# Optimization experiments

Hardware: AMD Instinct MI355X
Metric: run time of the kernel (lower is better)

## Reference

```python
import jax, jax.numpy as jnp
import numpy as np

NUM_EXPERTS = 64
TOP_K = 2
NOISE_EPS = 0.01


def setup_inputs() -> dict:
    key = jax.random.key(0)
    k1, k2, k3, k4 = jax.random.split(key, 4)
    B, D, E = 32768, 2048, NUM_EXPERTS
    x = jax.random.normal(k1, (B, D), dtype=jnp.float32)
    # original inits these to zero; use small random weights for a non-degenerate top-k
    w_gate = jax.random.normal(k2, (D, E), dtype=jnp.float32) * 0.02
    w_noise = jax.random.normal(k3, (D, E), dtype=jnp.float32) * 0.02
    noise = jax.random.normal(k4, (B, E), dtype=jnp.float32)  # tf.random.normal draw, fixed
    return {"x": x, "w_gate": w_gate, "w_noise": w_noise, "noise": noise}


def reference(x, w_gate, w_noise, noise):
    # routing_pooling='flatten' on a 2D input is identity
    pooled = x  # [B, D]
    routing = pooled @ w_gate  # [B, E]
    # noisy routing (training=True path)
    noise_stddev = jax.nn.softplus(pooled @ w_noise) + NOISE_EPS
    routing = routing + noise * noise_stddev
    # softmax_top_k: take top k+1, keep top k, softmax, scatter back to E experts
    kk = min(TOP_K + 1, NUM_EXPERTS)
    top_vals, top_idx = jax.lax.top_k(routing, kk)
    top_k_vals = top_vals[:, :TOP_K]            # [B, k]
    top_k_idx = top_idx[:, :TOP_K]              # [B, k]
    top_k_gates = jax.nn.softmax(top_k_vals, axis=-1)
    B = routing.shape[0]
    rows = jnp.arange(B)[:, None]
    # rowwise_unsorted_segment_sum -> scatter gates into expert slots
    out = jnp.zeros((B, NUM_EXPERTS), dtype=routing.dtype).at[rows, top_k_idx].add(top_k_gates)
    return out
```

## Files before the change

### kernel.cpp

```cpp
#include <hip/hip_runtime.h>
#include <math.h>


typedef _Float16 half4v __attribute__((ext_vector_type(4)));
typedef _Float16 half8v __attribute__((ext_vector_type(8)));
typedef float f32x4 __attribute__((ext_vector_type(4)));

constexpr int DIMK = 2048;
constexpr int NEXP = 64;
constexpr int BM   = 64;
constexpr int NCH  = DIMK / 32;

__device__ __forceinline__ void async_load16(const void* g, void* l) {
    __builtin_amdgcn_global_load_lds(
        (const __attribute__((address_space(1))) unsigned int*)g,
        (__attribute__((address_space(3))) unsigned int*)l, 16, 0, 0);
}

__device__ __forceinline__ bool gt_pair(float a, int ia, float b, int ib) {
    return (a > b) || (a == b && ia < ib);
}

__global__ __launch_bounds__(256)
void presplit_kernel(const float* __restrict__ wg, const float* __restrict__ wn,
                     _Float16* __restrict__ wsB)
{
    int gid  = blockIdx.x * 256 + threadIdx.x;
    int lane = gid & 63;
    int t    = (gid >> 6) & 7;
    int c    = gid >> 9;
    int n    = t * 16 + (lane & 15);
    int kb   = c * 32 + ((lane >> 4) << 3);
    const float* src = (n < NEXP) ? (wg + n) : (wn + (n - NEXP));
    half8v h1, h2;
    #pragma unroll
    for (int j = 0; j < 8; ++j) {
        float w = src[(size_t)(kb + j) * NEXP] * 65536.0f;
        _Float16 a = (_Float16)w;
        h1[j] = a;
        h2[j] = (_Float16)(w - (float)a);
    }
    *(half8v*)(wsB + ((((size_t)c * 2 + 0) * 8 + t) * 64 + lane) * 8) = h1;
    *(half8v*)(wsB + ((((size_t)c * 2 + 1) * 8 + t) * 64 + lane) * 8) = h2;
}

__global__ __launch_bounds__(256)
void routing_mfma(const float* __restrict__ x, const _Float16* __restrict__ wsB,
                  const float* __restrict__ noise, float* __restrict__ out)
{
    __shared__ _Float16 Bp[4][2][8][64][8];
    __shared__ float4   cand[BM][2];
    __shared__ float4   res[BM];

    const int tid  = threadIdx.x;
    const int lane = tid & 63;
    const int w    = tid >> 6;
    const int wm   = w >> 1;
    const int wnh  = w & 1;
    const int q    = lane >> 4;
    const int cidx = lane & 15;
    const int row0 = blockIdx.x * BM;

    f32x4  acc[2][4] = {};
    float4 ra[2][4];

    const float* xr0 = x + (size_t)(row0 + wm * 32 + cidx) * DIMK + q * 8;
    const float* xr1 = xr0 + 16 * DIMK;

    auto issue_B = [&](int c, int buf) {
        #pragma unroll
        for (int ii = 0; ii < 4; ++ii) {
            int idx = w * 4 + ii;
            int p = idx >> 3, t = idx & 7;
            const _Float16* g = wsB + ((((size_t)c * 2 + p) * 8 + t) * 64 + lane) * 8;
            async_load16(g, &Bp[buf][p][t][0][0]);
        }
    };

#define ISSUE_A(C, S)                                            \
    {   const float* pa_ = xr0 + (C) * 32;                       \
        const float* pb_ = xr1 + (C) * 32;                       \
        ra[S][0] = *(const float4*)(pa_);                        \
        ra[S][1] = *(const float4*)(pa_ + 4);                    \
        ra[S][2] = *(const float4*)(pb_);                        \
        ra[S][3] = *(const float4*)(pb_ + 4);  }

#define FENCE() asm volatile("" ::: "memory")

#define STEP(C, BUF, NBUF, SEL, ISS, WN)                                     \
    {                                                                        \
        asm volatile("s_waitcnt vmcnt(" #WN ")" ::: "memory");               \
        asm volatile("s_barrier" ::: "memory");                              \
        if (ISS) issue_B((C) + 2, NBUF);                                     \
        half8v af[2][2];                                                     \
        _Pragma("unroll")                                                    \
        for (int mt = 0; mt < 2; ++mt) {                                     \
            _Pragma("unroll")                                                \
            for (int h = 0; h < 2; ++h) {                                    \
                float4 v = ra[SEL][mt * 2 + h];                              \
                float f0 = v.x * 1024.f, f1 = v.y * 1024.f;                  \
                float f2 = v.z * 1024.f, f3 = v.w * 1024.f;                  \
                _Float16 a0 = (_Float16)f0, a1 = (_Float16)f1;               \
                _Float16 a2 = (_Float16)f2, a3 = (_Float16)f3;               \
                af[mt][0][h * 4 + 0] = a0;                                   \
                af[mt][0][h * 4 + 1] = a1;                                   \
                af[mt][0][h * 4 + 2] = a2;                                   \
                af[mt][0][h * 4 + 3] = a3;                                   \
                af[mt][1][h * 4 + 0] = (_Float16)(f0 - (float)a0);           \
                af[mt][1][h * 4 + 1] = (_Float16)(f1 - (float)a1);           \
                af[mt][1][h * 4 + 2] = (_Float16)(f2 - (float)a2);           \
                af[mt][1][h * 4 + 3] = (_Float16)(f3 - (float)a3);           \
            }                                                                \
        }                                                                    \
        if (ISS) ISSUE_A((C) + 2, SEL);                                      \
        half8v bf[4][2];                                                     \
        _Pragma("unroll")                                                    \
        for (int tt = 0; tt < 4; ++tt) {                                     \
            int ntile = (tt < 2) ? (wnh * 2 + tt) : (4 + wnh * 2 + (tt - 2));\
            _Pragma("unroll")                                                \
            for (int p = 0; p < 2; ++p)                                      \
                bf[tt][p] = *(const half8v*)&Bp[BUF][p][ntile][lane][0];     \
        }                                                                    \
        _Pragma("unroll")                                                    \
        for (int mt = 0; mt < 2; ++mt) {                                     \
            _Pragma("unroll")                                                \
            for (int tt = 0; tt < 4; ++tt) {                                 \
                acc[mt][tt] = __builtin_amdgcn_mfma_f32_16x16x32_f16(        \
                    af[mt][0], bf[tt][0], acc[mt][tt], 0, 0, 0);             \
                acc[mt][tt] = __builtin_amdgcn_mfma_f32_16x16x32_f16(        \
                    af[mt][0], bf[tt][1], acc[mt][tt], 0, 0, 0);             \
                acc[mt][tt] = __builtin_amdgcn_mfma_f32_16x16x32_f16(        \
                    af[mt][1], bf[tt][0], acc[mt][tt], 0, 0, 0);             \
            }                                                                \
        }                                                                    \
    }

    issue_B(0, 0);
    ISSUE_A(0, 0);
    FENCE();
    issue_B(1, 1);
    ISSUE_A(1, 1);

    #pragma unroll 1
    for (int cb = 0; cb < NCH - 4; cb += 4) {
        STEP(cb + 0, 0, 2, 0, 1, 8)
        STEP(cb + 1, 1, 3, 1, 1, 8)
        STEP(cb + 2, 2, 0, 0, 1, 8)
        STEP(cb + 3, 3, 1, 1, 1, 8)
    }
    STEP(NCH - 4, 0, 2, 0, 1, 8)
    STEP(NCH - 3, 1, 3, 1, 1, 8)
    STEP(NCH - 2, 2, 0, 0, 0, 8)
    STEP(NCH - 1, 3, 0, 1, 0, 0)

#undef STEP
#undef ISSUE_A
#undef FENCE

    const float s = 0x1p-26f;
    #pragma unroll
    for (int mt = 0; mt < 2; ++mt) {
        float rv[2][4];
        #pragma unroll
        for (int g = 0; g < 2; ++g) {
            int e     = wnh * 32 + g * 16 + cidx;
            int rbase = row0 + wm * 32 + mt * 16 + q * 4;
            #pragma unroll
            for (int r = 0; r < 4; ++r) {
                float nz   = noise[(size_t)(rbase + r) * NEXP + e];
                float gate = acc[mt][g][r] * s;
                float nv   = acc[mt][g + 2][r] * s;
                float sp   = fmaxf(nv, 0.f) + log1pf(expf(-fabsf(nv)));
                rv[g][r]   = gate + nz * (sp + 0.01f);
            }
        }
        #pragma unroll
        for (int r = 0; r < 4; ++r) {
            int e0 = wnh * 32 + cidx, e1 = e0 + 16;
            float v1, v2; int i1, i2;
            float a = rv[0][r], b = rv[1][r];
            if (a >= b) { v1 = a; i1 = e0; v2 = b; i2 = e1; }
            else        { v1 = b; i1 = e1; v2 = a; i2 = e0; }
            #pragma unroll
            for (int m = 1; m <= 8; m <<= 1) {
                float b1 = __shfl_xor(v1, m); int ib1 = __shfl_xor(i1, m);
                float b2 = __shfl_xor(v2, m); int ib2 = __shfl_xor(i2, m);
                if (gt_pair(b1, ib1, v1, i1)) {
                    float o1 = v1; int oi1 = i1;
                    v1 = b1; i1 = ib1;
                    if (gt_pair(b2, ib2, o1, oi1)) { v2 = b2; i2 = ib2; }
                    else                           { v2 = o1; i2 = oi1; }
                } else if (gt_pair(b1, ib1, v2, i2)) {
                    v2 = b1; i2 = ib1;
                }
            }
            if (cidx == 0) {
                int rowb = wm * 32 + mt * 16 + q * 4 + r;
                cand[rowb][wnh] = make_float4(v1, __int_as_float(i1),
                                              v2, __int_as_float(i2));
            }
        }
    }
    __syncthreads();

    if (tid < BM) {
        float4 c0 = cand[tid][0], c1 = cand[tid][1];
        float mv1 = c0.x; int mi1 = __float_as_int(c0.y);
        float mv2 = c0.z; int mi2 = __float_as_int(c0.w);
        float b1 = c1.x;  int ib1 = __float_as_int(c1.y);
        float b2 = c1.z;  int ib2 = __float_as_int(c1.w);
        if (gt_pair(b1, ib1, mv1, mi1)) {
            float o1 = mv1; int oi1 = mi1;
            mv1 = b1; mi1 = ib1;
            if (gt_pair(b2, ib2, o1, oi1)) { mv2 = b2; mi2 = ib2; }
            else                           { mv2 = o1; mi2 = oi1; }
        } else if (gt_pair(b1, ib1, mv2, mi2)) {
            mv2 = b1; mi2 = ib1;
        }
        float t  = expf(mv2 - mv1);
        float g1 = 1.f / (1.f + t);
        res[tid] = make_float4(g1, __int_as_float(mi1),
                               t * g1, __int_as_float(mi2));
    }
    __syncthreads();

    {
        int rr  = tid >> 2;
        int seg = tid & 3;
        float4 rv = res[rr];
        float g1 = rv.x, g2 = rv.z;
        int   j1 = __float_as_int(rv.y), j2 = __float_as_int(rv.w);
        float* op = out + (size_t)(row0 + rr) * NEXP + seg * 16;
        #pragma unroll
        for (int qq = 0; qq < 4; ++qq) {
            int e0 = seg * 16 + qq * 4;
            float4 o;
            o.x = (e0 + 0 == j1) ? g1 : ((e0 + 0 == j2) ? g2 : 0.f);
            o.y = (e0 + 1 == j1) ? g1 : ((e0 + 1 == j2) ? g2 : 0.f);
            o.z = (e0 + 2 == j1) ? g1 : ((e0 + 2 == j2) ? g2 : 0.f);
            o.w = (e0 + 3 == j1) ? g1 : ((e0 + 3 == j2) ? g2 : 0.f);
            *(float4*)(op + qq * 4) = o;
        }
    }
}

extern "C" void kernel_launch(void* const* d_in, const int* in_sizes, int n_in,
                              void* d_out, int out_size, void* d_ws, size_t ws_size,
                              hipStream_t stream) {
    const float* x     = (const float*)d_in[0];
    const float* wg    = (const float*)d_in[1];
    const float* wn    = (const float*)d_in[2];
    const float* noise = (const float*)d_in[3];
    float* out = (float*)d_out;
    _Float16* wsB = (_Float16*)d_ws;

    presplit_kernel<<<dim3(128), 256, 0, stream>>>(wg, wn, wsB);

    const int Brows = in_sizes[0] / DIMK;
    dim3 grid(Brows / BM);
    routing_mfma<<<grid, 256, 0, stream>>>(x, wsB, noise, out);
}
```

Measured before the change: 419.3 us.

## Use 8 waves per block with one M-tile each and deeper prefetch

After: 403.3 us. 1.04x faster.

```diff
diff --git a/kernel.cpp b/kernel.cpp
--- a/kernel.cpp
+++ b/kernel.cpp
@@ -44,7 +44,7 @@
     *(half8v*)(wsB + ((((size_t)c * 2 + 1) * 8 + t) * 64 + lane) * 8) = h2;
 }
 
-__global__ __launch_bounds__(256)
+__global__ __launch_bounds__(512, 4)
 void routing_mfma(const float* __restrict__ x, const _Float16* __restrict__ wsB,
                   const float* __restrict__ noise, float* __restrict__ out)
 {
@@ -55,22 +55,21 @@
     const int tid  = threadIdx.x;
     const int lane = tid & 63;
     const int w    = tid >> 6;
-    const int wm   = w >> 1;
+    const int mt   = w >> 1;
     const int wnh  = w & 1;
     const int q    = lane >> 4;
     const int cidx = lane & 15;
     const int row0 = blockIdx.x * BM;
 
-    f32x4  acc[2][4] = {};
-    float4 ra[2][4];
-
-    const float* xr0 = x + (size_t)(row0 + wm * 32 + cidx) * DIMK + q * 8;
-    const float* xr1 = xr0 + 16 * DIMK;
+    f32x4  acc[4] = {};
+    float4 ra[4][2];
+
+    const float* xr0 = x + (size_t)(row0 + mt * 16 + cidx) * DIMK + q * 8;
 
     auto issue_B = [&](int c, int buf) {
         #pragma unroll
-        for (int ii = 0; ii < 4; ++ii) {
-            int idx = w * 4 + ii;
+        for (int ii = 0; ii < 2; ++ii) {
+            int idx = w * 2 + ii;
             int p = idx >> 3, t = idx & 7;
             const _Float16* g = wsB + ((((size_t)c * 2 + p) * 8 + t) * 64 + lane) * 8;
             async_load16(g, &Bp[buf][p][t][0][0]);
@@ -79,60 +78,46 @@
 
 #define ISSUE_A(C, S)                                            \
     {   const float* pa_ = xr0 + (C) * 32;                       \
-        const float* pb_ = xr1 + (C) * 32;                       \
         ra[S][0] = *(const float4*)(pa_);                        \
-        ra[S][1] = *(const float4*)(pa_ + 4);                    \
-        ra[S][2] = *(const float4*)(pb_);                        \
-        ra[S][3] = *(const float4*)(pb_ + 4);  }
+        ra[S][1] = *(const float4*)(pa_ + 4);  }
 
 #define FENCE() asm volatile("" ::: "memory")
 
-#define STEP(C, BUF, NBUF, SEL, ISS, WN)                                     \
+#define STEP(C, ISS, WN)                                                     \
     {                                                                        \
         asm volatile("s_waitcnt vmcnt(" #WN ")" ::: "memory");               \
         asm volatile("s_barrier" ::: "memory");                              \
-        if (ISS) issue_B((C) + 2, NBUF);                                     \
-        half8v af[2][2];                                                     \
+        if (ISS) issue_B((C) + 3, ((C) + 3) & 3);                            \
+        half8v af0, af1;                                                     \
         _Pragma("unroll")                                                    \
-        for (int mt = 0; mt < 2; ++mt) {                                     \
-            _Pragma("unroll")                                                \
-            for (int h = 0; h < 2; ++h) {                                    \
-                float4 v = ra[SEL][mt * 2 + h];                              \
-                float f0 = v.x * 1024.f, f1 = v.y * 1024.f;                  \
-                float f2 = v.z * 1024.f, f3 = v.w * 1024.f;                  \
-                _Float16 a0 = (_Float16)f0, a1 = (_Float16)f1;               \
-                _Float16 a2 = (_Float16)f2, a3 = (_Float16)f3;               \
-                af[mt][0][h * 4 + 0] = a0;                                   \
-                af[mt][0][h * 4 + 1] = a1;                                   \
-                af[mt][0][h * 4 + 2] = a2;                                   \
-                af[mt][0][h * 4 + 3] = a3;                                   \
-                af[mt][1][h * 4 + 0] = (_Float16)(f0 - (float)a0);           \
-                af[mt][1][h * 4 + 1] = (_Float16)(f1 - (float)a1);           \
-                af[mt][1][h * 4 + 2] = (_Float16)(f2 - (float)a2);           \
-                af[mt][1][h * 4 + 3] = (_Float16)(f3 - (float)a3);           \
-            }                                                                \
+        for (int h = 0; h < 2; ++h) {                                        \
+            float4 v = ra[(C) & 3][h];                                       \
+            float f0 = v.x * 1024.f, f1 = v.y * 1024.f;                      \
+            float f2 = v.z * 1024.f, f3 = v.w * 1024.f;                      \
+            _Float16 a0 = (_Float16)f0, a1 = (_Float16)f1;                   \
+            _Float16 a2 = (_Float16)f2, a3 = (_Float16)f3;                   \
+            af0[h * 4 + 0] = a0; af0[h * 4 + 1] = a1;                        \
+            af0[h * 4 + 2] = a2; af0[h * 4 + 3] = a3;                        \
+            af1[h * 4 + 0] = (_Float16)(f0 - (float)a0);                     \
+            af1[h * 4 + 1] = (_Float16)(f1 - (float)a1);                     \
+            af1[h * 4 + 2] = (_Float16)(f2 - (float)a2);                     \
+            af1[h * 4 + 3] = (_Float16)(f3 - (float)a3);                     \
         }                                                                    \
-        if (ISS) ISSUE_A((C) + 2, SEL);                                      \
-        half8v bf[4][2];                                                     \
+        if (ISS) ISSUE_A((C) + 3, ((C) + 3) & 3);                            \
+        __builtin_amdgcn_s_setprio(1);                                       \
         _Pragma("unroll")                                                    \
         for (int tt = 0; tt < 4; ++tt) {                                     \
             int ntile = (tt < 2) ? (wnh * 2 + tt) : (4 + wnh * 2 + (tt - 2));\
-            _Pragma("unroll")                                                \
-            for (int p = 0; p < 2; ++p)                                      \
-                bf[tt][p] = *(const half8v*)&Bp[BUF][p][ntile][lane][0];     \
+            half8v b0 = *(const half8v*)&Bp[(C) & 3][0][ntile][lane][0];     \
+            half8v b1 = *(const half8v*)&Bp[(C) & 3][1][ntile][lane][0];     \
+            acc[tt] = __builtin_amdgcn_mfma_f32_16x16x32_f16(                \
+                af0, b0, acc[tt], 0, 0, 0);                                  \
+            acc[tt] = __builtin_amdgcn_mfma_f32_16x16x32_f16(                \
+                af0, b1, acc[tt], 0, 0, 0);                                  \
+            acc[tt] = __builtin_amdgcn_mfma_f32_16x16x32_f16(                \
+                af1, b0, acc[tt], 0, 0, 0);                                  \
         }                                                                    \
-        _Pragma("unroll")                                                    \
-        for (int mt = 0; mt < 2; ++mt) {                                     \
-            _Pragma("unroll")                                                \
-            for (int tt = 0; tt < 4; ++tt) {                                 \
-                acc[mt][tt] = __builtin_amdgcn_mfma_f32_16x16x32_f16(        \
-                    af[mt][0], bf[tt][0], acc[mt][tt], 0, 0, 0);             \
-                acc[mt][tt] = __builtin_amdgcn_mfma_f32_16x16x32_f16(        \
-                    af[mt][0], bf[tt][1], acc[mt][tt], 0, 0, 0);             \
-                acc[mt][tt] = __builtin_amdgcn_mfma_f32_16x16x32_f16(        \
-                    af[mt][1], bf[tt][0], acc[mt][tt], 0, 0, 0);             \
-            }                                                                \
-        }                                                                    \
+        __builtin_amdgcn_s_setprio(0);                                       \
     }
 
     issue_B(0, 0);
@@ -140,36 +125,38 @@
     FENCE();
     issue_B(1, 1);
     ISSUE_A(1, 1);
+    FENCE();
+    issue_B(2, 2);
+    ISSUE_A(2, 2);
 
     #pragma unroll 1
     for (int cb = 0; cb < NCH - 4; cb += 4) {
-        STEP(cb + 0, 0, 2, 0, 1, 8)
-        STEP(cb + 1, 1, 3, 1, 1, 8)
-        STEP(cb + 2, 2, 0, 0, 1, 8)
-        STEP(cb + 3, 3, 1, 1, 1, 8)
-    }
-    STEP(NCH - 4, 0, 2, 0, 1, 8)
-    STEP(NCH - 3, 1, 3, 1, 1, 8)
-    STEP(NCH - 2, 2, 0, 0, 0, 8)
-    STEP(NCH - 1, 3, 0, 1, 0, 0)
+        STEP(cb + 0, 1, 8)
+        STEP(cb + 1, 1, 8)
+        STEP(cb + 2, 1, 8)
+        STEP(cb + 3, 1, 8)
+    }
+    STEP(NCH - 4, 1, 8)
+    STEP(NCH - 3, 0, 8)
+    STEP(NCH - 2, 0, 4)
+    STEP(NCH - 1, 0, 0)
 
 #undef STEP
 #undef ISSUE_A
 #undef FENCE
 
     const float s = 0x1p-26f;
-    #pragma unroll
-    for (int mt = 0; mt < 2; ++mt) {
+    {
         float rv[2][4];
+        const int rbase = row0 + mt * 16 + q * 4;
         #pragma unroll
         for (int g = 0; g < 2; ++g) {
-            int e     = wnh * 32 + g * 16 + cidx;
-            int rbase = row0 + wm * 32 + mt * 16 + q * 4;
+            int e = wnh * 32 + g * 16 + cidx;
             #pragma unroll
             for (int r = 0; r < 4; ++r) {
                 float nz   = noise[(size_t)(rbase + r) * NEXP + e];
-                float gate = acc[mt][g][r] * s;
-                float nv   = acc[mt][g + 2][r] * s;
+                float gate = acc[g][r] * s;
+                float nv   = acc[g + 2][r] * s;
                 float sp   = fmaxf(nv, 0.f) + log1pf(expf(-fabsf(nv)));
                 rv[g][r]   = gate + nz * (sp + 0.01f);
             }
@@ -195,7 +182,7 @@
                 }
             }
             if (cidx == 0) {
-                int rowb = wm * 32 + mt * 16 + q * 4 + r;
+                int rowb = mt * 16 + q * 4 + r;
                 cand[rowb][wnh] = make_float4(v1, __int_as_float(i1),
                                               v2, __int_as_float(i2));
             }
@@ -225,15 +212,15 @@
     __syncthreads();
 
     {
-        int rr  = tid >> 2;
-        int seg = tid & 3;
+        int rr  = tid >> 3;
+        int seg = tid & 7;
         float4 rv = res[rr];
         float g1 = rv.x, g2 = rv.z;
         int   j1 = __float_as_int(rv.y), j2 = __float_as_int(rv.w);
-        float* op = out + (size_t)(row0 + rr) * NEXP + seg * 16;
-        #pragma unroll
-        for (int qq = 0; qq < 4; ++qq) {
-            int e0 = seg * 16 + qq * 4;
+        float* op = out + (size_t)(row0 + rr) * NEXP + seg * 8;
+        #pragma unroll
+        for (int qq = 0; qq < 2; ++qq) {
+            int e0 = seg * 8 + qq * 4;
             float4 o;
             o.x = (e0 + 0 == j1) ? g1 : ((e0 + 0 == j2) ? g2 : 0.f);
             o.y = (e0 + 1 == j1) ? g1 : ((e0 + 1 == j2) ? g2 : 0.f);
@@ -258,5 +245,5 @@
 
     const int Brows = in_sizes[0] / DIMK;
     dim3 grid(Brows / BM);
-    routing_mfma<<<grid, 256, 0, stream>>>(x, wsB, noise, out);
-}
+    routing_mfma<<<grid, 512, 0, stream>>>(x, wsB, noise, out);
+}
```
